# Kernel tuning notes

Hardware: AMD Instinct MI355X
Metric: run time of the kernel (lower is better)

Reference implementation:

```python
import jax, jax.numpy as jnp
import numpy as np

N_HEADS = 8
FACTOR = 5


def setup_inputs() -> dict:
    key = jax.random.key(0)
    ks = jax.random.split(key, 8)
    B, L, D = 2, 4096, 512
    sample_k = min(FACTOR * int(np.ceil(np.log(L))), L)  # 45
    inp = {
        "queries": jax.random.normal(ks[0], (B, L, D), jnp.float32),
        "keys": jax.random.normal(ks[1], (B, L, D), jnp.float32),
        "values": jax.random.normal(ks[2], (B, L, D), jnp.float32),
        "Wq": jax.random.normal(ks[3], (D, D), jnp.float32) * 0.02,
        "bq": jnp.zeros((D,), jnp.float32),
        "Wk": jax.random.normal(ks[4], (D, D), jnp.float32) * 0.02,
        "bk": jnp.zeros((D,), jnp.float32),
        "Wv": jax.random.normal(ks[5], (D, D), jnp.float32) * 0.02,
        "bv": jnp.zeros((D,), jnp.float32),
        "index_sample": jax.random.randint(ks[6], (L, sample_k), 0, L, jnp.int32),
    }
    return inp


def reference(queries, keys, values, Wq, bq, Wk, bk, Wv, bv, index_sample):
    b, l_q, d_model = queries.shape
    _, l_k, _ = keys.shape
    h = N_HEADS
    d = d_model // h
    # projections -> [b, h, l, d]
    q = (queries @ Wq + bq).reshape(b, l_q, h, d).transpose(0, 2, 1, 3)
    k = (keys @ Wk + bk).reshape(b, l_k, h, d).transpose(0, 2, 1, 3)
    v = (values @ Wv + bv).reshape(b, l_k, h, d).transpose(0, 2, 1, 3)
    n_top = min(FACTOR * int(np.ceil(np.log(l_q))), l_q)
    # --- prob_qk: sparse sampled QK ---
    # gather sampled keys per query position: [b, h, l_q, sample_k, d]
    k_sample = k[:, :, index_sample, :]
    q_k_sample = jnp.einsum('bhld,bhlsd->bhls', q, k_sample)
    # sparsity measure M(q, K) = max - mean
    m = q_k_sample.max(-1) - q_k_sample.sum(-1) / l_k  # [b, h, l_q]
    _, m_top = jax.lax.top_k(m, n_top)  # [b, h, n_top]
    q_reduce = jnp.take_along_axis(q, m_top[..., None], axis=2)  # [b, h, u, d]
    scores = jnp.einsum('bhud,bhkd->bhuk', q_reduce, k)  # [b, h, u, l_k]
    scale = float(1.0 / np.sqrt(d))
    scores = scores * scale
    # --- causal ProbMask on the selected query rows ---
    causal = jnp.triu(jnp.ones((l_q, l_k), bool), 1)
    mask = causal[m_top]  # [b, h, u, l_k]
    scores = jnp.where(mask, -jnp.inf, scores)
    attn = jax.nn.softmax(scores, axis=-1)
    # --- initial context: causal cumsum of V; scatter updated rows ---
    context = jnp.cumsum(v, axis=2)  # [b, h, l_q, d]
    upd = jnp.einsum('bhuk,bhkd->bhud', attn, v)
    bi = jnp.arange(b)[:, None, None]
    hi = jnp.arange(h)[None, :, None]
    context = context.at[bi, hi, m_top].set(upd)
    return context.transpose(0, 2, 1, 3).reshape(b, l_q, h * d)
```

## Files before the change

kernel.cpp:

```cpp
#include <hip/hip_runtime.h>
#include <math.h>

#define B  2
#define L  4096
#define D  512
#define H  8
#define DH 64
#define BH (B * H)
#define K3 1536
#define XPW 1024

typedef short s16x8 __attribute__((ext_vector_type(8)));
typedef float f32x4 __attribute__((ext_vector_type(4)));

#define AS1 __attribute__((address_space(1)))
#define AS3 __attribute__((address_space(3)))

__device__ __forceinline__ void lds_load16(const void* g, void* l) {
    __builtin_amdgcn_global_load_lds((const AS1 unsigned int*)g,
                                     (AS3 unsigned int*)l, 16, 0, 0);
}

__device__ __forceinline__ unsigned short f2bf(float x) {
    union { float f; unsigned u; } v; v.f = x;
    unsigned u = v.u;
    return (unsigned short)((u + 0x7fff + ((u >> 16) & 1)) >> 16);
}
__device__ __forceinline__ float bf2f(unsigned short h) {
    union { float f; unsigned u; } v; v.u = ((unsigned)h) << 16;
    return v.f;
}

__global__ __launch_bounds__(256)
void k_split(const float* __restrict__ q, const float* __restrict__ k,
             const float* __restrict__ v,
             const float* __restrict__ wq, const float* __restrict__ wk,
             const float* __restrict__ wv,
             unsigned short* __restrict__ Xp, unsigned short* __restrict__ WpT)
{
    const int tid = threadIdx.x;
    if (blockIdx.x < 192) {
        __shared__ float t[64][65];
        const int bx = blockIdx.x;
        const int e  = bx >> 6;
        const int k0 = (bx & 7) * 64;
        const int n0 = ((bx >> 3) & 7) * 64;
        const float* W = (e == 0) ? wq : (e == 1) ? wk : wv;

        for (int idx = tid; idx < 64 * 16; idx += 256) {
            const int i = idx >> 4, j4 = (idx & 15) << 2;
            *(float4*)&t[i][j4] = *(const float4*)(W + (size_t)(k0 + i) * 512 + n0 + j4);
        }
        __syncthreads();

        const int n_loc = tid >> 2;
        const int kq    = (tid & 3) << 4;
        unsigned short h[16], l[16];
        #pragma unroll
        for (int tt = 0; tt < 16; tt++) {
            const float x = t[kq + tt][n_loc];
            h[tt] = f2bf(x);
            l[tt] = f2bf(x - bf2f(h[tt]));
        }
        unsigned short* base = WpT + (size_t)e * 512 * K3 + (size_t)(n0 + n_loc) * K3 + k0 + kq;
        #pragma unroll
        for (int g4 = 0; g4 < 4; g4++) {
            ushort4 hv = make_ushort4(h[g4*4], h[g4*4+1], h[g4*4+2], h[g4*4+3]);
            ushort4 lv = make_ushort4(l[g4*4], l[g4*4+1], l[g4*4+2], l[g4*4+3]);
            *(ushort4*)(base + g4*4)        = hv;
            *(ushort4*)(base + 512 + g4*4)  = lv;
            *(ushort4*)(base + 1024 + g4*4) = hv;
        }
    } else {
        const size_t g = (size_t)(blockIdx.x - 192) * 256 + tid;
        const size_t per = (size_t)8192 * 128;
        const int e = (int)(g / per);
        const size_t rem = g - (size_t)e * per;
        const int m  = (int)(rem >> 7);
        const int kq = (int)(rem & 127) << 2;

        const float* X = (e == 0) ? q : (e == 1) ? k : v;
        const float4 x = *(const float4*)(X + (size_t)m * 512 + kq);

        unsigned short h0 = f2bf(x.x), h1 = f2bf(x.y), h2 = f2bf(x.z), h3 = f2bf(x.w);
        unsigned short* dst = Xp + (size_t)e * 8192 * XPW + (size_t)m * XPW + kq;
        *(ushort4*)(dst) = make_ushort4(h0, h1, h2, h3);
        if (e != 2) {
            unsigned short l0 = f2bf(x.x - bf2f(h0)), l1 = f2bf(x.y - bf2f(h1));
            unsigned short l2 = f2bf(x.z - bf2f(h2)), l3 = f2bf(x.w - bf2f(h3));
            *(ushort4*)(dst + 512) = make_ushort4(l0, l1, l2, l3);
        }
    }
}

__global__ __launch_bounds__(256)
void gemm_mfma(const unsigned short* __restrict__ Xp,
               const unsigned short* __restrict__ WpT,
               const float* __restrict__ bq, const float* __restrict__ bk,
               const float* __restrict__ bv,
               float* __restrict__ Qo, float* __restrict__ Ko,
               float* __restrict__ Vo)
{
    __shared__ __align__(16) unsigned short smA[4096];
    __shared__ __align__(16) unsigned short smB[4096];

    const int e = blockIdx.z;
    const float* bias = (e == 0) ? bq : (e == 1) ? bk : bv;
    float* C          = (e == 0) ? Qo : (e == 1) ? Ko : Vo;
    const unsigned short* Ag = Xp  + (size_t)e * 8192 * XPW;
    const unsigned short* Bg = WpT + (size_t)e * 512 * K3;
    const int kEnd = (e == 2) ? 512 : K3;

    const int tid  = threadIdx.x;
    const int lane = tid & 63;
    const int wid  = tid >> 6;
    const int wm   = wid & 1;
    const int wn   = wid >> 1;
    const int m0   = blockIdx.x * 128;
    const int n0g  = blockIdx.y * 128;

    const int r1 = tid >> 2;
    const int c8 = (((tid & 3) ^ ((r1 >> 1) & 3)) << 3);
    const unsigned short* agp = Ag + (size_t)(m0 + r1) * XPW + c8;
    const unsigned short* bgp = Bg + (size_t)(n0g + r1) * K3 + c8;
    unsigned short* lA1 = smA + (size_t)(tid & ~63) * 8;
    unsigned short* lA2 = lA1 + 2048;
    unsigned short* lB1 = smB + (size_t)(tid & ~63) * 8;
    unsigned short* lB2 = lB1 + 2048;

    const int r    = lane & 15;
    const int quad = lane >> 4;
    const int swz  = ((quad ^ ((lane >> 1) & 3)) << 4);
    const char* pA = (const char*)smA + (wm * 64 + r) * 64 + swz;
    const char* pB = (const char*)smB + (wn * 64 + r) * 64 + swz;

    f32x4 acc[4][4];
    #pragma unroll
    for (int i = 0; i < 4; i++)
        #pragma unroll
        for (int j = 0; j < 4; j++)
            acc[i][j] = (f32x4){0.f, 0.f, 0.f, 0.f};

    for (int k0 = 0; k0 < kEnd; k0 += 32) {
        const int kA = (k0 < 512) ? k0 : k0 - 512;
        lds_load16(agp + kA, lA1);
        lds_load16(agp + (size_t)64 * XPW + kA, lA2);
        lds_load16(bgp + k0, lB1);
        lds_load16(bgp + (size_t)64 * K3 + k0, lB2);
        __syncthreads();

        s16x8 af[4], bf[4];
        #pragma unroll
        for (int mt = 0; mt < 4; mt++) af[mt] = *(const s16x8*)(pA + mt * 1024);
        #pragma unroll
        for (int nt = 0; nt < 4; nt++) bf[nt] = *(const s16x8*)(pB + nt * 1024);
        #pragma unroll
        for (int mt = 0; mt < 4; mt++)
            #pragma unroll
            for (int nt = 0; nt < 4; nt++)
                acc[mt][nt] = __builtin_amdgcn_mfma_f32_16x16x32_bf16(
                    af[mt], bf[nt], acc[mt][nt], 0, 0, 0);
        __syncthreads();
    }

    #pragma unroll
    for (int nt = 0; nt < 4; nt++) {
        const int col = n0g + wn * 64 + nt * 16 + r;
        const float bb = bias[col];
        #pragma unroll
        for (int mt = 0; mt < 4; mt++) {
            const int row0 = m0 + wm * 64 + mt * 16 + quad * 4;
            #pragma unroll
            for (int i = 0; i < 4; i++)
                C[(size_t)(row0 + i) * 512 + col] = acc[mt][nt][i] + bb;
        }
    }
}

#define CH 64
__global__ __launch_bounds__(256)
void k_sample_chunks(const float* __restrict__ Q, const float* __restrict__ K,
                     const int* __restrict__ idx, float* __restrict__ m_out, int S,
                     const float* __restrict__ V, float* __restrict__ partial)
{
    const int tid = threadIdx.x;
    if (blockIdx.x < 256) {
        const int bid = blockIdx.x;
        const int c  = (bid & 15) * 4 + (tid >> 6);
        const int h  = (bid >> 4) & (H - 1);
        const int b  = bid >> 7;
        const int d  = tid & 63;
        const float* base = V + (size_t)b * L * D + h * DH + d + (size_t)(c * CH) * D;

        float vals[CH];
        #pragma unroll
        for (int i = 0; i < CH; i++) vals[i] = base[(size_t)i * D];

        float s0 = 0.f, s1 = 0.f, s2 = 0.f, s3 = 0.f;
        #pragma unroll
        for (int i = 0; i < CH; i += 4) {
            s0 += vals[i]; s1 += vals[i+1]; s2 += vals[i+2]; s3 += vals[i+3];
        }
        partial[((size_t)((b * H + h) * 64 + c)) * DH + d] = (s0 + s1) + (s2 + s3);
    } else {
        __shared__ float qs[4][DH];
        const int lane = tid & 63;
        const int wib  = tid >> 6;
        const int i    = blockIdx.x - 256;
        const int bh   = i & 15;
        const int lg   = i >> 4;
        const int l = lg * 4 + wib;
        const int h = bh & (H - 1);
        const int b = bh >> 3;
        const int wid = (bh << 12) | l;

        qs[wib][lane] = Q[((size_t)b * L + l) * D + h * DH + lane];
        __syncthreads();

        const int r4 = lane >> 2;
        const int c4 = lane & 3;

        float4 qf[4];
        {
            const float4* qv = (const float4*)qs[wib];
            #pragma unroll
            for (int ii = 0; ii < 4; ii++) qf[ii] = qv[c4 + 4 * ii];
        }

        const float* Kb = K + (size_t)b * L * D + h * DH;
        const int* is = idx + (size_t)l * S;

        float vmax = -INFINITY, vsum = 0.f;
        const int passes = (S + 15) >> 4;
        for (int p = 0; p < passes; p++) {
            const int sp = p * 16 + r4;
            const bool ok = sp < S;
            const int j = ok ? is[sp] : 0;
            const float4* Krow = (const float4*)(Kb + (size_t)j * D);
            float dot = 0.f;
            #pragma unroll
            for (int ii = 0; ii < 4; ii++) {
                const float4 kv = Krow[c4 + 4 * ii];
                const float4 qq = qf[ii];
                dot += qq.x * kv.x + qq.y * kv.y + qq.z * kv.z + qq.w * kv.w;
            }
            dot += __shfl_xor(dot, 1, 64);
            dot += __shfl_xor(dot, 2, 64);
            if (ok) {
                vmax = fmaxf(vmax, dot);
                if (c4 == 0) vsum += dot;
            }
        }
        #pragma unroll
        for (int off = 32; off; off >>= 1) {
            vmax = fmaxf(vmax, __shfl_xor(vmax, off, 64));
            vsum += __shfl_xor(vsum, off, 64);
        }
        if (lane == 0) m_out[wid] = vmax - vsum * (1.0f / (float)L);
    }
}

__global__ __launch_bounds__(256)
void topk_kernel(const float* __restrict__ m_in, int* __restrict__ m_top,
                 float* __restrict__ sums, int* __restrict__ flags, int NT)
{
    __shared__ unsigned hist[256];
    __shared__ unsigned sfx[257];
    __shared__ int sh_b, sh_rem;
    __shared__ int cnt_gt, cnt_eq;
    __shared__ int eqlist[128];

    const float* m = m_in + (size_t)blockIdx.x * L;
    const int tid = threadIdx.x;
    int* out = m_top + blockIdx.x * NT;
    int* fl  = flags + (size_t)blockIdx.x * L;

    if (tid < NT) sums[blockIdx.x * NT + tid] = 0.f;
    for (int i = tid; i < L; i += 256) fl[i] = 0;

    unsigned uv[16];
    #pragma unroll
    for (int k = 0; k < 16; k++) {
        const float f = m[tid + k * 256];
        const unsigned x = __float_as_uint(f);
        uv[k] = (x & 0x80000000u) ? ~x : (x | 0x80000000u);
    }

    unsigned prefix = 0;
    int rem = NT;

    for (int level = 0; level < 4; level++) {
        const int shift = 24 - level * 8;
        hist[tid] = 0;
        if (tid == 0) { cnt_gt = 0; cnt_eq = 0; }
        __syncthreads();
        #pragma unroll
        for (int k = 0; k < 16; k++) {
            const bool part = (level == 0) || ((uv[k] >> (shift + 8)) == prefix);
            if (part) atomicAdd(&hist[(uv[k] >> shift) & 255], 1u);
        }
        __syncthreads();
        if (tid < 64) {
            const unsigned s0 = hist[4*tid+0], s1 = hist[4*tid+1];
            const unsigned s2 = hist[4*tid+2], s3 = hist[4*tid+3];
            const unsigned loc = s0 + s1 + s2 + s3;
            unsigned suf = loc;
            #pragma unroll
            for (int off = 1; off < 64; off <<= 1) {
                const unsigned t = __shfl_down(suf, off, 64);
                if (tid + off < 64) suf += t;
            }
            const unsigned tail = suf - loc;
            sfx[4*tid+3] = tail + s3;
            sfx[4*tid+2] = tail + s3 + s2;
            sfx[4*tid+1] = tail + s3 + s2 + s1;
            sfx[4*tid+0] = suf;
            if (tid == 0) sfx[256] = 0;
        }
        __syncthreads();
        if (sfx[tid + 1] < (unsigned)rem && (unsigned)rem <= sfx[tid]) {
            sh_b   = tid;
            sh_rem = rem - (int)sfx[tid + 1];
        }
        __syncthreads();
        prefix = (prefix << 8) | (unsigned)sh_b;
        rem    = sh_rem;
        __syncthreads();
    }

    const unsigned T = prefix;
    const int n_gt = NT - rem;

    #pragma unroll
    for (int k = 0; k < 16; k++) {
        if (uv[k] > T) {
            const int pos = atomicAdd(&cnt_gt, 1);
            out[pos] = tid + k * 256;
        } else if (uv[k] == T) {
            const int pos = atomicAdd(&cnt_eq, 1);
            if (pos < 128) eqlist[pos] = tid + k * 256;
        }
    }
    __syncthreads();
    if (tid == 0) {
        int n = cnt_eq < 128 ? cnt_eq : 128;
        for (int r = 0; r < rem; r++) {
            int best = 0x7fffffff, bi = 0;
            for (int i = 0; i < n; i++)
                if (eqlist[i] < best) { best = eqlist[i]; bi = i; }
            out[n_gt + r] = best;
            eqlist[bi] = 0x7fffffff;
        }
    }
    __syncthreads();
    if (tid < NT) fl[out[tid]] = 1;
}

__global__ __launch_bounds__(256)
void k_cumsum_scores(const float* __restrict__ V, const float* __restrict__ partial,
                     const int* __restrict__ flags, float* __restrict__ out,
                     const float* __restrict__ Q, const float* __restrict__ K,
                     const int* __restrict__ m_top, float* __restrict__ scores,
                     float* __restrict__ sums, int NT)
{
    const int tid = threadIdx.x;
    if (blockIdx.x < 256) {
        const int bid = blockIdx.x;
        const int c  = (bid & 15) * 4 + (tid >> 6);
        const int h  = (bid >> 4) & (H - 1);
        const int b  = bid >> 7;
        const int d  = tid & 63;
        const size_t off = (size_t)b * L * D + h * DH + d + (size_t)(c * CH) * D;
        const float* base  = V   + off;
        float*       obase = out + off;
        const float* pb = partial + (size_t)((b * H + h) * 64) * DH + d;
        const int*   fp = flags + (size_t)(b * H + h) * L + c * CH;

        float vals[CH];
        #pragma unroll
        for (int i = 0; i < CH; i++) vals[i] = base[(size_t)i * D];

        float acc = 0.f;
        for (int cc = 0; cc < c; cc++) acc += pb[cc * DH];

        #pragma unroll
        for (int i = 0; i < CH; i++) {
            acc += vals[i];
            obase[(size_t)i * D] = fp[i] ? 0.f : acc;
        }
    } else {
        __shared__ float qsh[15][DH];
        __shared__ int   psh[15];

        const int rem2 = blockIdx.x - 256;
        const int bh = rem2 / 24;
        const int r2 = rem2 % 24;
        const int ug = r2 >> 3;
        const int jc = r2 & 7;
        const int h  = bh & (H - 1);
        const int b  = bh >> 3;
        const int j0 = jc * 512;

        for (int i = tid; i < 15 * DH; i += 256) {
            const int u = i >> 6, d = i & 63;
            const int p = m_top[bh * NT + ug * 15 + u];
            if (d == 0) psh[u] = p;
            qsh[u][d] = Q[((size_t)b * L + p) * D + h * DH + d];
        }
        __syncthreads();

        const float* Kb = K + (size_t)b * L * D + h * DH;
        const int ja = j0 + tid;
        const int jb = ja + 256;
        float4 k0[16], k1[16];
        {
            const float4* ra = (const float4*)(Kb + (size_t)ja * D);
            const float4* rb = (const float4*)(Kb + (size_t)jb * D);
            #pragma unroll
            for (int i = 0; i < 16; i++) { k0[i] = ra[i]; k1[i] = rb[i]; }
        }

        for (int u = 0; u < 15; u++) {
            const int p = psh[u];
            const float4* qv = (const float4*)qsh[u];
            float d0 = 0.f, d1 = 0.f;
            #pragma unroll
            for (int i = 0; i < 16; i++) {
                const float4 q4 = qv[i];
                d0 += q4.x * k0[i].x + q4.y * k0[i].y + q4.z * k0[i].z + q4.w * k0[i].w;
                d1 += q4.x * k1[i].x + q4.y * k1[i].y + q4.z * k1[i].z + q4.w * k1[i].w;
            }
            const float e0 = (ja <= p) ? __expf(d0 * 0.125f) : 0.f;
            const float e1 = (jb <= p) ? __expf(d1 * 0.125f) : 0.f;
            float* srow = scores + (size_t)(bh * NT + ug * 15 + u) * L;
            srow[ja] = e0;
            srow[jb] = e1;
            float t = e0 + e1;
            #pragma unroll
            for (int off = 32; off; off >>= 1) t += __shfl_xor(t, off, 64);
            if ((tid & 63) == 0) atomicAdd(&sums[bh * NT + ug * 15 + u], t);
        }
    }
}

__global__ __launch_bounds__(256)
void attn_wv(const float* __restrict__ scores, const float* __restrict__ V,
             const int* __restrict__ m_top, const float* __restrict__ sums,
             float* __restrict__ out, int NT)
{
    __shared__ float ssh[45][64];
    __shared__ float sinv[45];
    __shared__ int   psh[45];

    const int bh = blockIdx.y;
    const int h  = bh & (H - 1);
    const int b  = bh >> 3;
    const int j0 = blockIdx.x * 64;
    const int tid = threadIdx.x;
    const int d   = tid & 63;
    const int w   = tid >> 6;

    if (tid < NT) {
        psh[tid]  = m_top[bh * NT + tid];
        sinv[tid] = 1.0f / sums[bh * NT + tid];
    }

    const float* Vb = V + (size_t)b * L * D + h * DH + d;
    float vreg[64];
    #pragma unroll
    for (int i = 0; i < 64; i++) vreg[i] = Vb[(size_t)(j0 + i) * D];

    __syncthreads();
    for (int i = tid; i < NT * 64; i += 256) {
        const int u = i >> 6, j = i & 63;
        ssh[u][j] = scores[(size_t)(bh * NT + u) * L + j0 + j] * sinv[u];
    }
    __syncthreads();

    for (int u = w; u < NT; u += 4) {
        const int p = psh[u];
        if (p < j0) continue;
        const float* wt = ssh[u];
        float acc = 0.f;
        #pragma unroll
        for (int i = 0; i < 64; i++) acc += wt[i] * vreg[i];
        atomicAdd(out + ((size_t)b * L + p) * D + h * DH + d, acc);
    }
}

extern "C" void kernel_launch(void* const* d_in, const int* in_sizes, int n_in,
                              void* d_out, int out_size, void* d_ws, size_t ws_size,
                              hipStream_t stream)
{
    const float* queries = (const float*)d_in[0];
    const float* keys    = (const float*)d_in[1];
    const float* values  = (const float*)d_in[2];
    const float* Wq      = (const float*)d_in[3];
    const float* bq      = (const float*)d_in[4];
    const float* Wk      = (const float*)d_in[5];
    const float* bk      = (const float*)d_in[6];
    const float* Wv      = (const float*)d_in[7];
    const float* bv      = (const float*)d_in[8];
    const int*   idx     = (const int*)d_in[9];
    float* out = (float*)d_out;

    const int S  = in_sizes[9] / L;
    const int NT = S;

    const size_t NE = (size_t)B * L * D;
    float* Qb      = (float*)d_ws;
    float* Kb      = Qb + NE;
    float* Vb      = Kb + NE;
    float* m_buf   = Vb + NE;
    float* cs_part = m_buf + (size_t)BH * L;
    int*   m_top   = (int*)(cs_part + (size_t)BH * 64 * DH);
    float* sums    = (float*)(m_top + 1024);
    int*   flags   = (int*)(sums + 1024);
    float* scores  = (float*)(flags + (size_t)BH * L);
    unsigned short* Xp  = (unsigned short*)(scores + (size_t)BH * NT * L);
    unsigned short* WpT = Xp + (size_t)3 * 8192 * XPW;

    k_split<<<192 + 3 * 8192 * 128 / 256, 256, 0, stream>>>(
        queries, keys, values, Wq, Wk, Wv, Xp, WpT);

    gemm_mfma<<<dim3(8192 / 128, 512 / 128, 3), 256, 0, stream>>>(
        Xp, WpT, bq, bk, bv, Qb, Kb, Vb);

    k_sample_chunks<<<256 + BH * L / 4, 256, 0, stream>>>(
        Qb, Kb, idx, m_buf, S, Vb, cs_part);

    topk_kernel<<<BH, 256, 0, stream>>>(m_buf, m_top, sums, flags, NT);

    k_cumsum_scores<<<256 + 384, 256, 0, stream>>>(
        Vb, cs_part, flags, out, Qb, Kb, m_top, scores, sums, NT);

    attn_wv<<<dim3(64, BH), 256, 0, stream>>>(scores, Vb, m_top, sums, out, NT);
}
```

Baseline: 270.5 us.

## Rewrite projection GEMM as 256x256 tile, 8-wave double-buffered pipeline

The projection GEMM moves from 128x128 tiles with 4 waves and single-buffered K=32 steps to 256x256 tiles with 8 waves. It now uses double-buffered K=64 LDS stages with an XOR swizzle, and prefetches the next A and B tiles while the MFMAs run. It also uses explicit vmcnt/lgkmcnt waits, raw s_barrier and s_setprio to interleave loads with compute. The aim is better data reuse and to hide global-to-LDS latency. In exchange the grid becomes much smaller (192 blocks) with 128KB of LDS per block, which limits occupancy and may underfill the CUs.

```diff
diff --git a/kernel.cpp b/kernel.cpp
--- a/kernel.cpp
+++ b/kernel.cpp
@@ -29,6 +29,13 @@
 __device__ __forceinline__ float bf2f(unsigned short h) {
     union { float f; unsigned u; } v; v.u = ((unsigned)h) << 16;
     return v.f;
+}
+
+#define MEMFENCE asm volatile("" ::: "memory")
+__device__ __forceinline__ void wg_bar() {
+    MEMFENCE;
+    __builtin_amdgcn_s_barrier();
+    MEMFENCE;
 }
 
 __global__ __launch_bounds__(256)
@@ -93,7 +100,9 @@
     }
 }
 
-__global__ __launch_bounds__(256)
+#define MFMA16 __builtin_amdgcn_mfma_f32_16x16x32_bf16
+
+__global__ __launch_bounds__(512, 2)
 void gemm_mfma(const unsigned short* __restrict__ Xp,
                const unsigned short* __restrict__ WpT,
                const float* __restrict__ bq, const float* __restrict__ bk,
@@ -101,75 +110,150 @@
                float* __restrict__ Qo, float* __restrict__ Ko,
                float* __restrict__ Vo)
 {
-    __shared__ __align__(16) unsigned short smA[4096];
-    __shared__ __align__(16) unsigned short smB[4096];
+    __shared__ __align__(16) unsigned short lds[65536];
 
     const int e = blockIdx.z;
     const float* bias = (e == 0) ? bq : (e == 1) ? bk : bv;
     float* C          = (e == 0) ? Qo : (e == 1) ? Ko : Vo;
     const unsigned short* Ag = Xp  + (size_t)e * 8192 * XPW;
     const unsigned short* Bg = WpT + (size_t)e * 512 * K3;
-    const int kEnd = (e == 2) ? 512 : K3;
+    const int NT = (e == 2) ? 8 : 24;
 
     const int tid  = threadIdx.x;
     const int lane = tid & 63;
     const int wid  = tid >> 6;
     const int wm   = wid & 1;
     const int wn   = wid >> 1;
-    const int m0   = blockIdx.x * 128;
-    const int n0g  = blockIdx.y * 128;
-
-    const int r1 = tid >> 2;
-    const int c8 = (((tid & 3) ^ ((r1 >> 1) & 3)) << 3);
-    const unsigned short* agp = Ag + (size_t)(m0 + r1) * XPW + c8;
-    const unsigned short* bgp = Bg + (size_t)(n0g + r1) * K3 + c8;
-    unsigned short* lA1 = smA + (size_t)(tid & ~63) * 8;
-    unsigned short* lA2 = lA1 + 2048;
-    unsigned short* lB1 = smB + (size_t)(tid & ~63) * 8;
-    unsigned short* lB2 = lB1 + 2048;
-
-    const int r    = lane & 15;
-    const int quad = lane >> 4;
-    const int swz  = ((quad ^ ((lane >> 1) & 3)) << 4);
-    const char* pA = (const char*)smA + (wm * 64 + r) * 64 + swz;
-    const char* pB = (const char*)smB + (wn * 64 + r) * 64 + swz;
-
-    f32x4 acc[4][4];
+    const int m0   = blockIdx.x * 256;
+    const int n0g  = blockIdx.y * 256;
+
+    const int srow = wid * 8 + (lane >> 3);
+    const int scq8 = ((lane & 7) ^ (lane >> 3)) << 3;
+    const unsigned short* aSrc = Ag + (size_t)(m0 + srow) * XPW + scq8;
+    const unsigned short* bSrc = Bg + (size_t)(n0g + srow) * K3 + scq8;
+    unsigned short* ldsA = lds;
+    unsigned short* ldsB = lds + 32768;
+    unsigned short* dA = ldsA + wid * 512;
+    unsigned short* dB = ldsB + wid * 512;
+
+    const int r16 = lane & 15, quad = lane >> 4;
+    const int x3 = r16 & 7;
+    const int c0 = ((quad ^ x3) << 4);
+    const int c1 = (((4 | quad) ^ x3) << 4);
+    const char* fA = (const char*)ldsA + (wm * 128 + r16) * 128;
+    const char* fB = (const char*)ldsB + (wn * 64 + r16) * 128;
+
+    f32x4 acc[8][4];
     #pragma unroll
-    for (int i = 0; i < 4; i++)
+    for (int i = 0; i < 8; i++)
         #pragma unroll
         for (int j = 0; j < 4; j++)
             acc[i][j] = (f32x4){0.f, 0.f, 0.f, 0.f};
 
-    for (int k0 = 0; k0 < kEnd; k0 += 32) {
-        const int kA = (k0 < 512) ? k0 : k0 - 512;
-        lds_load16(agp + kA, lA1);
-        lds_load16(agp + (size_t)64 * XPW + kA, lA2);
-        lds_load16(bgp + k0, lB1);
-        lds_load16(bgp + (size_t)64 * K3 + k0, lB2);
-        __syncthreads();
-
-        s16x8 af[4], bf[4];
-        #pragma unroll
-        for (int mt = 0; mt < 4; mt++) af[mt] = *(const s16x8*)(pA + mt * 1024);
-        #pragma unroll
-        for (int nt = 0; nt < 4; nt++) bf[nt] = *(const s16x8*)(pB + nt * 1024);
-        #pragma unroll
-        for (int mt = 0; mt < 4; mt++)
-            #pragma unroll
-            for (int nt = 0; nt < 4; nt++)
-                acc[mt][nt] = __builtin_amdgcn_mfma_f32_16x16x32_bf16(
-                    af[mt], bf[nt], acc[mt][nt], 0, 0, 0);
-        __syncthreads();
+    #pragma unroll
+    for (int j = 0; j < 4; j++)
+        lds_load16(aSrc + (size_t)(j * 64) * XPW, dA + j * 4096);
+    #pragma unroll
+    for (int j = 0; j < 4; j++)
+        lds_load16(bSrc + (size_t)(j * 64) * K3, dB + j * 4096);
+
+    s16x8 aF[8], b0[4], b1[4];
+
+    for (int t = 0; t < NT; ++t) {
+        const int pa = (t & 1) << 15;
+        const int na = (~t & 1) * 16384;
+        if (t + 1 < NT) {
+            const int k1 = (t + 1) * 64;
+            const int ka = (k1 < 512) ? k1 : k1 - 512;
+            #pragma unroll
+            for (int j = 0; j < 4; j++)
+                lds_load16(aSrc + (size_t)(j * 64) * XPW + ka, dA + na + j * 4096);
+            asm volatile("s_waitcnt vmcnt(4)" ::: "memory");
+        } else {
+            asm volatile("s_waitcnt vmcnt(0)" ::: "memory");
+        }
+        wg_bar();
+        #pragma unroll
+        for (int mq = 0; mq < 4; mq++) {
+            aF[mq * 2]     = *(const s16x8*)(fA + pa + mq * 2048 + c0);
+            aF[mq * 2 + 1] = *(const s16x8*)(fA + pa + mq * 2048 + c1);
+        }
+        #pragma unroll
+        for (int nq = 0; nq < 2; nq++) {
+            b0[nq * 2]     = *(const s16x8*)(fB + pa + nq * 2048 + c0);
+            b0[nq * 2 + 1] = *(const s16x8*)(fB + pa + nq * 2048 + c1);
+        }
+        wg_bar();
+        asm volatile("s_waitcnt lgkmcnt(0)" ::: "memory");
+        __builtin_amdgcn_s_setprio(1);
+        #pragma unroll
+        for (int mq = 0; mq < 4; mq++)
+            #pragma unroll
+            for (int nq = 0; nq < 2; nq++) {
+                acc[mq][nq] = MFMA16(aF[mq*2],   b0[nq*2],   acc[mq][nq], 0, 0, 0);
+                acc[mq][nq] = MFMA16(aF[mq*2+1], b0[nq*2+1], acc[mq][nq], 0, 0, 0);
+            }
+        __builtin_amdgcn_s_setprio(0);
+        wg_bar();
+        if (t + 1 < NT) {
+            const int kb = (t + 1) * 64;
+            #pragma unroll
+            for (int j = 0; j < 4; j++)
+                lds_load16(bSrc + (size_t)(j * 64) * K3 + kb, dB + na + j * 4096);
+        }
+        #pragma unroll
+        for (int nq = 0; nq < 2; nq++) {
+            b1[nq * 2]     = *(const s16x8*)(fB + pa + (2 + nq) * 2048 + c0);
+            b1[nq * 2 + 1] = *(const s16x8*)(fB + pa + (2 + nq) * 2048 + c1);
+        }
+        wg_bar();
+        asm volatile("s_waitcnt lgkmcnt(0)" ::: "memory");
+        __builtin_amdgcn_s_setprio(1);
+        #pragma unroll
+        for (int mq = 0; mq < 4; mq++)
+            #pragma unroll
+            for (int nq = 0; nq < 2; nq++) {
+                acc[mq][2+nq] = MFMA16(aF[mq*2],   b1[nq*2],   acc[mq][2+nq], 0, 0, 0);
+                acc[mq][2+nq] = MFMA16(aF[mq*2+1], b1[nq*2+1], acc[mq][2+nq], 0, 0, 0);
+            }
+        __builtin_amdgcn_s_setprio(0);
+        wg_bar();
+        #pragma unroll
+        for (int mq = 0; mq < 4; mq++) {
+            aF[mq * 2]     = *(const s16x8*)(fA + pa + 8192 + mq * 2048 + c0);
+            aF[mq * 2 + 1] = *(const s16x8*)(fA + pa + 8192 + mq * 2048 + c1);
+        }
+        wg_bar();
+        asm volatile("s_waitcnt lgkmcnt(0)" ::: "memory");
+        __builtin_amdgcn_s_setprio(1);
+        #pragma unroll
+        for (int mq = 0; mq < 4; mq++)
+            #pragma unroll
+            for (int nq = 0; nq < 2; nq++) {
+                acc[4+mq][2+nq] = MFMA16(aF[mq*2],   b1[nq*2],   acc[4+mq][2+nq], 0, 0, 0);
+                acc[4+mq][2+nq] = MFMA16(aF[mq*2+1], b1[nq*2+1], acc[4+mq][2+nq], 0, 0, 0);
+            }
+        __builtin_amdgcn_s_setprio(0);
+        wg_bar();
+        __builtin_amdgcn_s_setprio(1);
+        #pragma unroll
+        for (int mq = 0; mq < 4; mq++)
+            #pragma unroll
+            for (int nq = 0; nq < 2; nq++) {
+                acc[4+mq][nq] = MFMA16(aF[mq*2],   b0[nq*2],   acc[4+mq][nq], 0, 0, 0);
+                acc[4+mq][nq] = MFMA16(aF[mq*2+1], b0[nq*2+1], acc[4+mq][nq], 0, 0, 0);
+            }
+        __builtin_amdgcn_s_setprio(0);
+        wg_bar();
     }
 
     #pragma unroll
     for (int nt = 0; nt < 4; nt++) {
-        const int col = n0g + wn * 64 + nt * 16 + r;
+        const int col = n0g + wn * 64 + nt * 16 + r16;
         const float bb = bias[col];
         #pragma unroll
-        for (int mt = 0; mt < 4; mt++) {
-            const int row0 = m0 + wm * 64 + mt * 16 + quad * 4;
+        for (int mt = 0; mt < 8; mt++) {
+            const int row0 = m0 + wm * 128 + mt * 16 + quad * 4;
             #pragma unroll
             for (int i = 0; i < 4; i++)
                 C[(size_t)(row0 + i) * 512 + col] = acc[mt][nt][i] + bb;
@@ -523,7 +607,7 @@
     k_split<<<192 + 3 * 8192 * 128 / 256, 256, 0, stream>>>(
         queries, keys, values, Wq, Wk, Wv, Xp, WpT);
 
-    gemm_mfma<<<dim3(8192 / 128, 512 / 128, 3), 256, 0, stream>>>(
+    gemm_mfma<<<dim3(8192 / 256, 512 / 256, 3), 512, 0, stream>>>(
         Xp, WpT, bq, bk, bv, Qb, Kb, Vb);
 
     k_sample_chunks<<<256 + BH * L / 4, 256, 0, stream>>>(
```

After: 266.9 us. No clear change (-1.3%).
